# Optimization experiments

Measured on AMD Instinct MI355X. Metric: run time of the kernel, lower is better.

Reference implementation:

```python
import jax, jax.numpy as jnp
import numpy as np

TAU = 0.5  # temperature from init_kwargs


def _semi_loss(h1, h2):
    # GRACE-style InfoNCE: -log( e^{sim(i,i')/tau} / (sum_refl + sum_between - e^{sim(i,i)/tau}) )
    n1 = h1 / jnp.linalg.norm(h1, axis=1, keepdims=True)
    n2 = h2 / jnp.linalg.norm(h2, axis=1, keepdims=True)
    refl = jnp.exp((n1 @ n1.T) / TAU)   # [N, N]
    betw = jnp.exp((n1 @ n2.T) / TAU)   # [N, N]
    denom = refl.sum(axis=1) + betw.sum(axis=1) - jnp.diagonal(refl)
    return -jnp.log(jnp.diagonal(betw) / denom)


def _contrast(h1, h2):
    # forward_v1 with batch_size=0 (batched path is mathematically identical)
    return (0.5 * (_semi_loss(h1, h2) + _semi_loss(h2, h1))).mean()


def _proj(z, Wa, ba, Wb, bb):
    # fc_b(elu(fc_a(z))); torch Linear: y = x @ W.T + b
    return jax.nn.elu(z @ Wa.T + ba) @ Wb.T + bb


def setup_inputs() -> dict:
    key = jax.random.key(0)
    ks = jax.random.split(key, 11)
    N, A, B = 8192, 32, 32
    D = A * B
    s = 1.0 / np.sqrt(D)
    inp = {
        'ta': jax.random.normal(ks[0], (N, A, B), dtype=jnp.float32),
        'tb': jax.random.normal(ks[1], (N, A, B), dtype=jnp.float32),
        'W1': jax.random.uniform(ks[2], (D, D), jnp.float32, -s, s),
        'b1': jax.random.uniform(ks[3], (D,), jnp.float32, -s, s),
        'W2': jax.random.uniform(ks[4], (D, D), jnp.float32, -s, s),
        'b2': jax.random.uniform(ks[5], (D,), jnp.float32, -s, s),
        'W3': jax.random.uniform(ks[6], (D, D), jnp.float32, -s, s),
        'b3': jax.random.uniform(ks[7], (D,), jnp.float32, -s, s),
        'W4': jax.random.uniform(ks[8], (D, D), jnp.float32, -s, s),
        'b4': jax.random.uniform(ks[9], (D,), jnp.float32, -s, s),
        'w_r1': jnp.array([0.5], dtype=jnp.float32),
    }
    return inp


def reference(ta, tb, W1, b1, W2, b2, W3, b3, W4, b4, w_r1):
    N = ta.shape[0]
    # row view: [N, A*B]
    z1 = ta.reshape(N, -1)
    z2 = tb.reshape(N, -1)
    loss_row = _contrast(_proj(z1, W1, b1, W2, b2), _proj(z2, W1, b1, W2, b2))
    # column view: permute(0,2,1) then flatten -> [N, B*A]
    z1c = jnp.transpose(ta, (0, 2, 1)).reshape(N, -1)
    z2c = jnp.transpose(tb, (0, 2, 1)).reshape(N, -1)
    loss_col = _contrast(_proj(z1c, W3, b3, W4, b4), _proj(z2c, W3, b3, W4, b4))
    w_row = jnp.clip(w_r1[0], 0.0, 1.0)
    return w_row * loss_row + (1.0 - w_row) * loss_col
```

## Files before the change

kernel.cpp:

```cpp
#include <hip/hip_runtime.h>
#include <stdint.h>


typedef unsigned short u16;
typedef __attribute__((ext_vector_type(8))) __bf16 bf16x8;
typedef __attribute__((ext_vector_type(4))) float f32x4;

#define NS 8192
#define DD 1024

__device__ __forceinline__ float bf2f(u16 u) {
    union { uint32_t i; float f; } v; v.i = ((uint32_t)u) << 16; return v.f;
}
__device__ __forceinline__ u16 f2bf(float f) {
    union { float f; uint32_t i; } v; v.f = f;
    return (u16)((v.i + 0x7FFFu + ((v.i >> 16) & 1u)) >> 16);
}

__device__ __forceinline__ void gload16(const u16* g, u16* l) {
    __builtin_amdgcn_global_load_lds(
        (__attribute__((address_space(1))) void*)(uintptr_t)(g),
        (__attribute__((address_space(3))) void*)(uintptr_t)(l), 16, 0, 0);
}


__global__ __launch_bounds__(256) void conv_f2bf(const float* __restrict__ src,
                                                 u16* __restrict__ dst) {
    int i = (blockIdx.x * 256 + threadIdx.x) * 4;
    float4 v = *(const float4*)(src + i);
    ushort4 o;
    o.x = f2bf(v.x); o.y = f2bf(v.y); o.z = f2bf(v.z); o.w = f2bf(v.w);
    *(ushort4*)(dst + i) = o;
}

__global__ __launch_bounds__(256) void conv_cat(const float* __restrict__ a,
                                                const float* __restrict__ b,
                                                u16* __restrict__ Z) {
    size_t i = (size_t)(blockIdx.x * 256 + threadIdx.x) * 4;
    const size_t half = (size_t)NS * DD;
    const float* s = (i < half) ? (a + i) : (b + (i - half));
    float4 v = *(const float4*)s;
    ushort4 o;
    o.x = f2bf(v.x); o.y = f2bf(v.y); o.z = f2bf(v.z); o.w = f2bf(v.w);
    *(ushort4*)(Z + i) = o;
}

__global__ __launch_bounds__(256) void conv_col(const float* __restrict__ a,
                                                const float* __restrict__ b,
                                                u16* __restrict__ Z) {
    size_t i = (size_t)(blockIdx.x * 256 + threadIdx.x) * 4;
    const size_t half = (size_t)NS * DD;
    const float* src; size_t o;
    if (i < half) { src = a; o = i; } else { src = b; o = i - half; }
    size_t row = o >> 10;
    int j = (int)(o & 1023);
    int aI = j & 31, bI = j >> 5;
    const float* rp = src + (row << 10);
    ushort4 ov;
    ov.x = f2bf(rp[aI * 32 + bI]);
    ov.y = f2bf(rp[(aI + 1) * 32 + bI]);
    ov.z = f2bf(rp[(aI + 2) * 32 + bI]);
    ov.w = f2bf(rp[(aI + 3) * 32 + bI]);
    *(ushort4*)(Z + i) = ov;
}

template <int MODE>
__global__ __launch_bounds__(256) void gemm_bt(const u16* A, const u16* B,
                                               const float* __restrict__ bias,
                                               u16* __restrict__ out,
                                               float* __restrict__ S) {
    __shared__ alignas(16) u16 As[128 * 32];
    __shared__ alignas(16) u16 Bs[128 * 32];
    const int tid = threadIdx.x;

    int tm, tn;
    if (MODE == 2) {
        int x = blockIdx.x, y = blockIdx.y;
        if (y + x < 128) { tm = y;       tn = y + x; }
        else             { tm = 127 - y; tn = x - 1; }
    } else {
        tm = blockIdx.y; tn = blockIdx.x;
    }
    const size_t tileM = (size_t)tm * 128;
    const size_t tileN = (size_t)tn * 128;

    const u16* gA0 = A + (tileM + (tid >> 2)) * DD + (tid & 3) * 8;
    const u16* gA1 = gA0 + (size_t)64 * DD;
    const u16* gB0 = B + (tileN + (tid >> 2)) * DD + (tid & 3) * 8;
    const u16* gB1 = gB0 + (size_t)64 * DD;
    u16* lA0 = &As[tid * 8]; u16* lA1 = lA0 + 2048;
    u16* lB0 = &Bs[tid * 8]; u16* lB1 = lB0 + 2048;

    const int lane = tid & 63;
    const int wv = tid >> 6;
    const int wr = (wv >> 1) << 6;
    const int wc = (wv & 1) << 6;
    const int lr = lane & 15;
    const int lh = lane >> 4;

    const u16* aBase = &As[(wr + lr) * 32 + lh * 8];
    const u16* bBase = &Bs[(wc + lr) * 32 + lh * 8];

    f32x4 acc[4][4];
#pragma unroll
    for (int i = 0; i < 4; i++)
#pragma unroll
        for (int j = 0; j < 4; j++) acc[i][j] = (f32x4)0.0f;

    for (int k0 = 0; k0 < DD; k0 += 32) {
        gload16(gA0 + k0, lA0);
        gload16(gA1 + k0, lA1);
        gload16(gB0 + k0, lB0);
        gload16(gB1 + k0, lB1);
        __syncthreads();
        bf16x8 af[4], bfr[4];
#pragma unroll
        for (int rt = 0; rt < 4; rt++) af[rt] = *(const bf16x8*)(aBase + rt * 512);
#pragma unroll
        for (int ct = 0; ct < 4; ct++) bfr[ct] = *(const bf16x8*)(bBase + ct * 512);
#pragma unroll
        for (int rt = 0; rt < 4; rt++)
#pragma unroll
            for (int ct = 0; ct < 4; ct++)
                acc[rt][ct] = __builtin_amdgcn_mfma_f32_16x16x32_bf16(
                    af[rt], bfr[ct], acc[rt][ct], 0, 0, 0);
        __syncthreads();
    }

    if (MODE <= 1) {
        float bcol[4];
#pragma unroll
        for (int ct = 0; ct < 4; ct++) bcol[ct] = bias[tileN + wc + ct * 16 + lr];
#pragma unroll
        for (int rt = 0; rt < 4; rt++) {
#pragma unroll
            for (int r = 0; r < 4; r++) {
                size_t row = tileM + wr + rt * 16 + lh * 4 + r;
                u16* orow = out + row * DD + tileN + wc + lr;
#pragma unroll
                for (int ct = 0; ct < 4; ct++) {
                    float v = acc[rt][ct][r] + bcol[ct];
                    if (MODE == 0) v = v > 0.0f ? v : expm1f(v);
                    orow[ct * 16] = f2bf(v);
                }
            }
        }
    } else {
        const bool offdiag = (tm != tn);
        float colsum[4] = {0.f, 0.f, 0.f, 0.f};
#pragma unroll
        for (int rt = 0; rt < 4; rt++) {
#pragma unroll
            for (int r = 0; r < 4; r++) {
                float rs = 0.0f;
#pragma unroll
                for (int ct = 0; ct < 4; ct++) {
                    float e = __expf(2.0f * acc[rt][ct][r]);
                    rs += e;
                    colsum[ct] += e;
                }
                rs += __shfl_xor(rs, 1);
                rs += __shfl_xor(rs, 2);
                rs += __shfl_xor(rs, 4);
                rs += __shfl_xor(rs, 8);
                if (lr == 0) {
                    size_t row = tileM + wr + rt * 16 + lh * 4 + r;
                    atomicAdd(&S[row], rs);
                }
            }
        }
        if (offdiag) {
#pragma unroll
            for (int ct = 0; ct < 4; ct++) {
                float cs = colsum[ct];
                cs += __shfl_xor(cs, 16);
                cs += __shfl_xor(cs, 32);
                if (lh == 0) {
                    size_t col = tileN + wc + ct * 16 + lr;
                    atomicAdd(&S[col], cs);
                }
            }
        }
    }
}

__global__ __launch_bounds__(256) void normalize_kernel(u16* M) {
    __shared__ float red[4];
    const int tid = threadIdx.x;
    u16* row = M + ((size_t)blockIdx.x << 10);
    ushort4 v = ((const ushort4*)row)[tid];
    float x0 = bf2f(v.x), x1 = bf2f(v.y), x2 = bf2f(v.z), x3 = bf2f(v.w);
    float s = x0 * x0 + x1 * x1 + x2 * x2 + x3 * x3;
#pragma unroll
    for (int m = 1; m < 64; m <<= 1) s += __shfl_xor(s, m);
    if ((tid & 63) == 0) red[tid >> 6] = s;
    __syncthreads();
    float inv = rsqrtf(red[0] + red[1] + red[2] + red[3]);
    ushort4 o;
    o.x = f2bf(x0 * inv); o.y = f2bf(x1 * inv);
    o.z = f2bf(x2 * inv); o.w = f2bf(x3 * inv);
    ((ushort4*)row)[tid] = o;
}

__global__ __launch_bounds__(256) void diag_kernel(const u16* M, float* g12) {
    __shared__ float red[4];
    const int tid = threadIdx.x;
    const u16* r1 = M + ((size_t)blockIdx.x << 10);
    const u16* r2 = r1 + ((size_t)NS << 10);
    ushort4 a = ((const ushort4*)r1)[tid];
    ushort4 b = ((const ushort4*)r2)[tid];
    float s = bf2f(a.x) * bf2f(b.x) + bf2f(a.y) * bf2f(b.y) +
              bf2f(a.z) * bf2f(b.z) + bf2f(a.w) * bf2f(b.w);
#pragma unroll
    for (int m = 1; m < 64; m <<= 1) s += __shfl_xor(s, m);
    if ((tid & 63) == 0) red[tid >> 6] = s;
    __syncthreads();
    if (tid == 0) g12[blockIdx.x] = red[0] + red[1] + red[2] + red[3];
}

__global__ __launch_bounds__(256) void final_kernel(const float* Sr, const float* Sc,
                                                    const float* gr, const float* gc,
                                                    const float* w_r1, float* out) {
    __shared__ float red[16];
    const float E2 = 7.389056098930650f;
    float a = 0.f, b = 0.f, c = 0.f, d = 0.f;
    for (int i = threadIdx.x; i < 2 * NS; i += 256) {
        a += logf(Sr[i] - E2);
        b += logf(Sc[i] - E2);
    }
    for (int i = threadIdx.x; i < NS; i += 256) {
        c += gr[i];
        d += gc[i];
    }
#pragma unroll
    for (int m = 1; m < 64; m <<= 1) {
        a += __shfl_xor(a, m); b += __shfl_xor(b, m);
        c += __shfl_xor(c, m); d += __shfl_xor(d, m);
    }
    int w = threadIdx.x >> 6;
    if ((threadIdx.x & 63) == 0) {
        red[w] = a; red[4 + w] = b; red[8 + w] = c; red[12 + w] = d;
    }
    __syncthreads();
    if (threadIdx.x == 0) {
        a = red[0] + red[1] + red[2] + red[3];
        b = red[4] + red[5] + red[6] + red[7];
        c = red[8] + red[9] + red[10] + red[11];
        d = red[12] + red[13] + red[14] + red[15];
        float lr = a / (2.0f * NS) - 2.0f * c / NS;
        float lc = b / (2.0f * NS) - 2.0f * d / NS;
        float w0 = w_r1[0];
        w0 = fminf(fmaxf(w0, 0.0f), 1.0f);
        out[0] = w0 * lr + (1.0f - w0) * lc;
    }
}

extern "C" void kernel_launch(void* const* d_in, const int* in_sizes, int n_in,
                              void* d_out, int out_size, void* d_ws, size_t ws_size,
                              hipStream_t stream) {
    const float* ta = (const float*)d_in[0];
    const float* tb = (const float*)d_in[1];
    const float* W1 = (const float*)d_in[2];
    const float* b1 = (const float*)d_in[3];
    const float* W2 = (const float*)d_in[4];
    const float* b2 = (const float*)d_in[5];
    const float* W3 = (const float*)d_in[6];
    const float* b3 = (const float*)d_in[7];
    const float* W4 = (const float*)d_in[8];
    const float* b4 = (const float*)d_in[9];
    const float* wr = (const float*)d_in[10];
    float* out = (float*)d_out;

    char* p = (char*)d_ws;
    const size_t MAT = (size_t)2 * NS * DD * sizeof(u16);
    u16* Z = (u16*)p;  p += MAT;
    u16* T = (u16*)p;  p += MAT;
    u16* H = (u16*)p;  p += MAT;
    u16* Wb = (u16*)p; p += (size_t)4 * DD * DD * sizeof(u16);
    float* Sr = (float*)p;  p += 2 * NS * sizeof(float);
    float* Sc = (float*)p;  p += 2 * NS * sizeof(float);
    float* gr = (float*)p;  p += NS * sizeof(float);
    float* gc = (float*)p;  p += NS * sizeof(float);

    u16* Wb1 = Wb;
    u16* Wb2 = Wb + (size_t)DD * DD;
    u16* Wb3 = Wb + (size_t)2 * DD * DD;
    u16* Wb4 = Wb + (size_t)3 * DD * DD;

    conv_f2bf<<<1024, 256, 0, stream>>>(W1, Wb1);
    conv_f2bf<<<1024, 256, 0, stream>>>(W2, Wb2);
    conv_f2bf<<<1024, 256, 0, stream>>>(W3, Wb3);
    conv_f2bf<<<1024, 256, 0, stream>>>(W4, Wb4);
    hipMemsetAsync(Sr, 0, 4 * NS * sizeof(float), stream);

    conv_cat<<<16384, 256, 0, stream>>>(ta, tb, Z);
    gemm_bt<0><<<dim3(8, 128), 256, 0, stream>>>(Z, Wb1, b1, T, nullptr);
    gemm_bt<1><<<dim3(8, 128), 256, 0, stream>>>(T, Wb2, b2, H, nullptr);
    normalize_kernel<<<16384, 256, 0, stream>>>(H);
    diag_kernel<<<8192, 256, 0, stream>>>(H, gr);
    gemm_bt<2><<<dim3(129, 64), 256, 0, stream>>>(H, H, nullptr, nullptr, Sr);

    conv_col<<<16384, 256, 0, stream>>>(ta, tb, Z);
    gemm_bt<0><<<dim3(8, 128), 256, 0, stream>>>(Z, Wb3, b3, T, nullptr);
    gemm_bt<1><<<dim3(8, 128), 256, 0, stream>>>(T, Wb4, b4, H, nullptr);
    normalize_kernel<<<16384, 256, 0, stream>>>(H);
    diag_kernel<<<8192, 256, 0, stream>>>(H, gc);
    gemm_bt<2><<<dim3(129, 64), 256, 0, stream>>>(H, H, nullptr, nullptr, Sc);

    final_kernel<<<1, 256, 0, stream>>>(Sr, Sc, gr, gc, wr, out);
}
```

Before: 1.224 ms.

## Compute contrastive Gram matrix with FP8 MFMA instead of BF16

The normalize kernel now also writes an FP8 (e4m3) copy of the normalized embeddings into the scratch buffer T. A new gram_fp8 kernel computes the symmetric 16384x16384 similarity Gram with the 16x16x128 scaled FP8 MFMA, using 128-wide K tiles and an XOR-swizzled LDS layout, and keeps the same triangular tile mapping and exp/row/col-sum epilogue. This halves operand bytes and raises peak matrix throughput for the largest GEMM. The cost is FP8 rounding of unit-norm vectors feeding exp(2*sim), which may perturb the loss beyond tolerance.

Result: slower. 1.392 ms (+13.7%).

```diff
diff --git a/kernel.cpp b/kernel.cpp
--- a/kernel.cpp
+++ b/kernel.cpp
@@ -5,6 +5,7 @@
 typedef unsigned short u16;
 typedef __attribute__((ext_vector_type(8))) __bf16 bf16x8;
 typedef __attribute__((ext_vector_type(4))) float f32x4;
+typedef __attribute__((ext_vector_type(8))) int i32x8;
 
 #define NS 8192
 #define DD 1024
@@ -17,7 +18,7 @@
     return (u16)((v.i + 0x7FFFu + ((v.i >> 16) & 1u)) >> 16);
 }
 
-__device__ __forceinline__ void gload16(const u16* g, u16* l) {
+__device__ __forceinline__ void gload16(const void* g, void* l) {
     __builtin_amdgcn_global_load_lds(
         (__attribute__((address_space(1))) void*)(uintptr_t)(g),
         (__attribute__((address_space(3))) void*)(uintptr_t)(l), 16, 0, 0);
@@ -67,20 +68,12 @@
 template <int MODE>
 __global__ __launch_bounds__(256) void gemm_bt(const u16* A, const u16* B,
                                                const float* __restrict__ bias,
-                                               u16* __restrict__ out,
-                                               float* __restrict__ S) {
+                                               u16* __restrict__ out) {
     __shared__ alignas(16) u16 As[128 * 32];
     __shared__ alignas(16) u16 Bs[128 * 32];
     const int tid = threadIdx.x;
 
-    int tm, tn;
-    if (MODE == 2) {
-        int x = blockIdx.x, y = blockIdx.y;
-        if (y + x < 128) { tm = y;       tn = y + x; }
-        else             { tm = 127 - y; tn = x - 1; }
-    } else {
-        tm = blockIdx.y; tn = blockIdx.x;
-    }
+    const int tm = blockIdx.y, tn = blockIdx.x;
     const size_t tileM = (size_t)tm * 128;
     const size_t tileN = (size_t)tn * 128;
 
@@ -127,64 +120,134 @@
         __syncthreads();
     }
 
-    if (MODE <= 1) {
-        float bcol[4];
-#pragma unroll
-        for (int ct = 0; ct < 4; ct++) bcol[ct] = bias[tileN + wc + ct * 16 + lr];
+    float bcol[4];
+#pragma unroll
+    for (int ct = 0; ct < 4; ct++) bcol[ct] = bias[tileN + wc + ct * 16 + lr];
+#pragma unroll
+    for (int rt = 0; rt < 4; rt++) {
+#pragma unroll
+        for (int r = 0; r < 4; r++) {
+            size_t row = tileM + wr + rt * 16 + lh * 4 + r;
+            u16* orow = out + row * DD + tileN + wc + lr;
+#pragma unroll
+            for (int ct = 0; ct < 4; ct++) {
+                float v = acc[rt][ct][r] + bcol[ct];
+                if (MODE == 0) v = v > 0.0f ? v : expm1f(v);
+                orow[ct * 16] = f2bf(v);
+            }
+        }
+    }
+}
+
+__global__ __launch_bounds__(256) void gram_fp8(const uint8_t* __restrict__ M,
+                                                float* __restrict__ S) {
+    __shared__ alignas(16) uint8_t As[128 * 128];
+    __shared__ alignas(16) uint8_t Bs[128 * 128];
+    const int tid = threadIdx.x;
+
+    int x = blockIdx.x, y = blockIdx.y;
+    int tm, tn;
+    if (y + x < 128) { tm = y;       tn = y + x; }
+    else             { tm = 127 - y; tn = x - 1; }
+    const size_t tileM = (size_t)tm * 128;
+    const size_t tileN = (size_t)tn * 128;
+
+    const int r0 = tid >> 3;
+    const int c0 = (tid & 7) ^ (r0 & 7);
+    const uint8_t* gA = M + (tileM + r0) * DD + c0 * 16;
+    const uint8_t* gB = M + (tileN + r0) * DD + c0 * 16;
+    uint8_t* lA = As + tid * 16;
+    uint8_t* lB = Bs + tid * 16;
+
+    const int lane = tid & 63;
+    const int wv = tid >> 6;
+    const int wr = (wv >> 1) << 6;
+    const int wc = (wv & 1) << 6;
+    const int lr = lane & 15;
+    const int lh = lane >> 4;
+    const int e0 = ((2 * lh) ^ (lr & 7)) * 16;
+    const int e1 = ((2 * lh + 1) ^ (lr & 7)) * 16;
+
+    f32x4 acc[4][4];
+#pragma unroll
+    for (int i = 0; i < 4; i++)
+#pragma unroll
+        for (int j = 0; j < 4; j++) acc[i][j] = (f32x4)0.0f;
+
+    for (int k0 = 0; k0 < DD; k0 += 128) {
+#pragma unroll
+        for (int i = 0; i < 4; i++)
+            gload16(gA + (size_t)i * 32 * DD + k0, lA + i * 4096);
+#pragma unroll
+        for (int i = 0; i < 4; i++)
+            gload16(gB + (size_t)i * 32 * DD + k0, lB + i * 4096);
+        __syncthreads();
+
+        i32x8 bfr[4];
+#pragma unroll
+        for (int ct = 0; ct < 4; ct++) {
+            const uint8_t* bp = Bs + (wc + ct * 16 + lr) * 128;
+            uint4 lo = *(const uint4*)(bp + e0);
+            uint4 hi = *(const uint4*)(bp + e1);
+            bfr[ct] = (i32x8){(int)lo.x, (int)lo.y, (int)lo.z, (int)lo.w,
+                              (int)hi.x, (int)hi.y, (int)hi.z, (int)hi.w};
+        }
 #pragma unroll
         for (int rt = 0; rt < 4; rt++) {
-#pragma unroll
-            for (int r = 0; r < 4; r++) {
+            const uint8_t* ap = As + (wr + rt * 16 + lr) * 128;
+            uint4 lo = *(const uint4*)(ap + e0);
+            uint4 hi = *(const uint4*)(ap + e1);
+            i32x8 af = {(int)lo.x, (int)lo.y, (int)lo.z, (int)lo.w,
+                        (int)hi.x, (int)hi.y, (int)hi.z, (int)hi.w};
+#pragma unroll
+            for (int ct = 0; ct < 4; ct++)
+                acc[rt][ct] = __builtin_amdgcn_mfma_scale_f32_16x16x128_f8f6f4(
+                    af, bfr[ct], acc[rt][ct],
+                    0, 0,
+                    0, 0x7F7F7F7F,
+                    0, 0x7F7F7F7F);
+        }
+        __syncthreads();
+    }
+
+    const bool offdiag = (tm != tn);
+    float colsum[4] = {0.f, 0.f, 0.f, 0.f};
+#pragma unroll
+    for (int rt = 0; rt < 4; rt++) {
+#pragma unroll
+        for (int r = 0; r < 4; r++) {
+            float rs = 0.0f;
+#pragma unroll
+            for (int ct = 0; ct < 4; ct++) {
+                float e = __expf(2.0f * acc[rt][ct][r]);
+                rs += e;
+                colsum[ct] += e;
+            }
+            rs += __shfl_xor(rs, 1);
+            rs += __shfl_xor(rs, 2);
+            rs += __shfl_xor(rs, 4);
+            rs += __shfl_xor(rs, 8);
+            if (lr == 0) {
                 size_t row = tileM + wr + rt * 16 + lh * 4 + r;
-                u16* orow = out + row * DD + tileN + wc + lr;
-#pragma unroll
-                for (int ct = 0; ct < 4; ct++) {
-                    float v = acc[rt][ct][r] + bcol[ct];
-                    if (MODE == 0) v = v > 0.0f ? v : expm1f(v);
-                    orow[ct * 16] = f2bf(v);
-                }
+                atomicAdd(&S[row], rs);
             }
         }
-    } else {
-        const bool offdiag = (tm != tn);
-        float colsum[4] = {0.f, 0.f, 0.f, 0.f};
-#pragma unroll
-        for (int rt = 0; rt < 4; rt++) {
-#pragma unroll
-            for (int r = 0; r < 4; r++) {
-                float rs = 0.0f;
-#pragma unroll
-                for (int ct = 0; ct < 4; ct++) {
-                    float e = __expf(2.0f * acc[rt][ct][r]);
-                    rs += e;
-                    colsum[ct] += e;
-                }
-                rs += __shfl_xor(rs, 1);
-                rs += __shfl_xor(rs, 2);
-                rs += __shfl_xor(rs, 4);
-                rs += __shfl_xor(rs, 8);
-                if (lr == 0) {
-                    size_t row = tileM + wr + rt * 16 + lh * 4 + r;
-                    atomicAdd(&S[row], rs);
-                }
+    }
+    if (offdiag) {
+#pragma unroll
+        for (int ct = 0; ct < 4; ct++) {
+            float cs = colsum[ct];
+            cs += __shfl_xor(cs, 16);
+            cs += __shfl_xor(cs, 32);
+            if (lh == 0) {
+                size_t col = tileN + wc + ct * 16 + lr;
+                atomicAdd(&S[col], cs);
             }
         }
-        if (offdiag) {
-#pragma unroll
-            for (int ct = 0; ct < 4; ct++) {
-                float cs = colsum[ct];
-                cs += __shfl_xor(cs, 16);
-                cs += __shfl_xor(cs, 32);
-                if (lh == 0) {
-                    size_t col = tileN + wc + ct * 16 + lr;
-                    atomicAdd(&S[col], cs);
-                }
-            }
-        }
-    }
-}
-
-__global__ __launch_bounds__(256) void normalize_kernel(u16* M) {
+    }
+}
+
+__global__ __launch_bounds__(256) void normalize_kernel(u16* M, uint8_t* F) {
     __shared__ float red[4];
     const int tid = threadIdx.x;
     u16* row = M + ((size_t)blockIdx.x << 10);
@@ -196,10 +259,13 @@
     if ((tid & 63) == 0) red[tid >> 6] = s;
     __syncthreads();
     float inv = rsqrtf(red[0] + red[1] + red[2] + red[3]);
+    float y0 = x0 * inv, y1 = x1 * inv, y2 = x2 * inv, y3 = x3 * inv;
     ushort4 o;
-    o.x = f2bf(x0 * inv); o.y = f2bf(x1 * inv);
-    o.z = f2bf(x2 * inv); o.w = f2bf(x3 * inv);
+    o.x = f2bf(y0); o.y = f2bf(y1); o.z = f2bf(y2); o.w = f2bf(y3);
     ((ushort4*)row)[tid] = o;
+    int pk = __builtin_amdgcn_cvt_pk_fp8_f32(y0, y1, 0, false);
+    pk = __builtin_amdgcn_cvt_pk_fp8_f32(y2, y3, pk, true);
+    ((int*)(F + ((size_t)blockIdx.x << 10)))[tid] = pk;
 }
 
 __global__ __launch_bounds__(256) void diag_kernel(const u16* M, float* g12) {
@@ -286,6 +352,7 @@
     u16* Wb2 = Wb + (size_t)DD * DD;
     u16* Wb3 = Wb + (size_t)2 * DD * DD;
     u16* Wb4 = Wb + (size_t)3 * DD * DD;
+    uint8_t* Hf8 = (uint8_t*)T;
 
     conv_f2bf<<<1024, 256, 0, stream>>>(W1, Wb1);
     conv_f2bf<<<1024, 256, 0, stream>>>(W2, Wb2);
@@ -294,18 +361,18 @@
     hipMemsetAsync(Sr, 0, 4 * NS * sizeof(float), stream);
 
     conv_cat<<<16384, 256, 0, stream>>>(ta, tb, Z);
-    gemm_bt<0><<<dim3(8, 128), 256, 0, stream>>>(Z, Wb1, b1, T, nullptr);
-    gemm_bt<1><<<dim3(8, 128), 256, 0, stream>>>(T, Wb2, b2, H, nullptr);
-    normalize_kernel<<<16384, 256, 0, stream>>>(H);
+    gemm_bt<0><<<dim3(8, 128), 256, 0, stream>>>(Z, Wb1, b1, T);
+    gemm_bt<1><<<dim3(8, 128), 256, 0, stream>>>(T, Wb2, b2, H);
+    normalize_kernel<<<16384, 256, 0, stream>>>(H, Hf8);
     diag_kernel<<<8192, 256, 0, stream>>>(H, gr);
-    gemm_bt<2><<<dim3(129, 64), 256, 0, stream>>>(H, H, nullptr, nullptr, Sr);
+    gram_fp8<<<dim3(129, 64), 256, 0, stream>>>(Hf8, Sr);
 
     conv_col<<<16384, 256, 0, stream>>>(ta, tb, Z);
-    gemm_bt<0><<<dim3(8, 128), 256, 0, stream>>>(Z, Wb3, b3, T, nullptr);
-    gemm_bt<1><<<dim3(8, 128), 256, 0, stream>>>(T, Wb4, b4, H, nullptr);
-    normalize_kernel<<<16384, 256, 0, stream>>>(H);
+    gemm_bt<0><<<dim3(8, 128), 256, 0, stream>>>(Z, Wb3, b3, T);
+    gemm_bt<1><<<dim3(8, 128), 256, 0, stream>>>(T, Wb4, b4, H);
+    normalize_kernel<<<16384, 256, 0, stream>>>(H, Hf8);
     diag_kernel<<<8192, 256, 0, stream>>>(H, gc);
-    gemm_bt<2><<<dim3(129, 64), 256, 0, stream>>>(H, H, nullptr, nullptr, Sc);
+    gram_fp8<<<dim3(129, 64), 256, 0, stream>>>(Hf8, Sc);
 
     final_kernel<<<1, 256, 0, stream>>>(Sr, Sc, gr, gc, wr, out);
 }
```
